# Optimization experiments

Measured on AMD Instinct MI355X. Metric: run time of the kernel, lower is better.

## Reference

```python
import jax, jax.numpy as jnp
import numpy as np

N_STATE = 1024
N_HEAD = 16
H_DIM = N_STATE // N_HEAD  # 64
NUM_ROT = 32
BASE = 10000.0
B, S = 4, 8192


def setup_inputs() -> dict:
    key = jax.random.key(0)
    k1, k2, k3 = jax.random.split(key, 3)
    x = jax.random.normal(k1, (B, S, N_STATE), dtype=jnp.float32)
    # learned params (use non-trivial values so the math is exercised)
    thetas = 0.1 * jax.random.normal(k2, (NUM_ROT,), dtype=jnp.float32)
    rotation_matrix = jnp.eye(H_DIM, dtype=jnp.float32) + 0.02 * jax.random.normal(k3, (H_DIM, H_DIM), dtype=jnp.float32)
    # buffer: inv_freq = 1 / base^(arange(0, h_dim, 2)/h_dim)
    inv_freq = 1.0 / (BASE ** (jnp.arange(0, H_DIM, 2, dtype=jnp.float32) / H_DIM))
    return {"x": x, "thetas": thetas, "rotation_matrix": rotation_matrix, "inv_freq": inv_freq}


def reference(x, thetas, rotation_matrix, inv_freq):
    batch, seq_len, n_state = x.shape
    h_dim = rotation_matrix.shape[0]
    n_head = n_state // h_dim
    num_rot = thetas.shape[0]

    xf = x.reshape(-1, h_dim)  # [B*S*n_head, h_dim]
    # Sequential Givens rotations: x @ G_k only mixes columns i and j.
    for k in range(num_rot):
        i, j = k % h_dim, (k + 1) % h_dim
        c = jnp.cos(thetas[k])
        s = jnp.sin(thetas[k])
        xi, xj = xf[:, i], xf[:, j]
        xf = xf.at[:, i].set(xi * c + xj * s).at[:, j].set(-xi * s + xj * c)
    xf = xf @ rotation_matrix
    xr = xf.reshape(batch, seq_len, n_head, h_dim)

    # RoPE-style sin/cos mixing (split-even/odd, concat halves as in source)
    pos = jnp.arange(seq_len, dtype=jnp.float32)
    sinusoid = pos[:, None] * inv_freq[None, :]          # [S, h_dim/2]
    sin = jnp.sin(sinusoid)[None, :, None, :]            # [1,S,1,h_dim/2]
    cos = jnp.cos(sinusoid)[None, :, None, :]
    x1, x2 = xr[..., ::2], xr[..., 1::2]
    out = jnp.concatenate([x1 * cos - x2 * sin, x1 * sin + x2 * cos], axis=-1)
    return out.reshape(batch, seq_len, n_state)
```

## Files before the change

kernel.cpp:

```cpp
#include <hip/hip_runtime.h>
#include <hip/hip_bf16.h>


#define TOKENS_PER_WAVE 8
#define N_TILES 32768
#define N_BLOCKS (N_TILES / (4 * TOKENS_PER_WAVE))

typedef __attribute__((ext_vector_type(8))) short short8;
typedef __attribute__((ext_vector_type(4))) float f32x4;

__device__ __forceinline__ unsigned short f2bf_bits(float f) {
  return __bfloat16_as_ushort(__float2bfloat16(f));
}

__global__ __launch_bounds__(64) void prep_kernel(
    const float* __restrict__ thetas,
    const float* __restrict__ R,
    short* __restrict__ Bws) {
  const int t = threadIdx.x;
  float col[64];
#pragma unroll
  for (int d = 0; d < 64; ++d) col[d] = R[d * 64 + t];
#pragma unroll
  for (int k = 31; k >= 0; --k) {
    float th = thetas[k];
    float ck = cosf(th), sk = sinf(th);
    float a = col[k], b = col[k + 1];
    col[k]     = ck * a - sk * b;
    col[k + 1] = sk * a + ck * b;
  }
  __shared__ float Ml[64][64];
#pragma unroll
  for (int d = 0; d < 64; ++d) Ml[d][t] = col[d];
  __syncthreads();

  short8* Bp = (short8*)Bws;
  const int cb = t & 15, kg = t >> 4;
#pragma unroll
  for (int s = 0; s < 2; ++s) {
#pragma unroll
    for (int nt = 0; nt < 4; ++nt) {
      const int c2 = cb + 16 * nt;
      const int pc = (c2 < 32) ? (2 * c2) : (2 * (c2 - 32) + 1);
      short8 hf;
#pragma unroll
      for (int e = 0; e < 8; ++e) {
        const int k = s * 32 + kg * 8 + e;
        hf[e] = (short)f2bf_bits(Ml[k][pc]);
      }
      Bp[(s * 4 + nt) * 64 + t] = hf;
    }
  }
}

__global__ __launch_bounds__(256, 4) void rope_mfma(
    const float* __restrict__ x,
    const float* __restrict__ inv_freq,
    const short* __restrict__ Bws,
    float* __restrict__ out) {
  const int lane = threadIdx.x & 63;
  const int wid = threadIdx.x >> 6;
  const int cb = lane & 15;
  const int kg = lane >> 4;

  const int tile0 = ((int)blockIdx.x * 4 + wid) * TOKENS_PER_WAVE;

  __shared__ alignas(16) float stage[4][2][16 * 64];
  __shared__ alignas(16) short8 Btab[8 * 64];

  f32x4 pb[4];
  {
    const f32x4* xb = (const f32x4*)x + (size_t)tile0 * 256;
#pragma unroll
    for (int j = 0; j < 4; ++j) pb[j] = xb[j * 64 + lane];
  }

  {
    const f32x4* Bg = (const f32x4*)Bws;
    f32x4* Bl = (f32x4*)Btab;
    const int i = threadIdx.x;
    Bl[i] = Bg[i];
    Bl[i + 256] = Bg[i + 256];
  }
  __syncthreads();

  short8 bh[8];
#pragma unroll
  for (int i = 0; i < 8; ++i) bh[i] = Btab[i * 64 + lane];

  const float iv0 = inv_freq[cb];
  const float iv1 = inv_freq[cb + 16];

#pragma unroll
  for (int t = 0; t < TOKENS_PER_WAVE; ++t) {
    const int tile = tile0 + t;
    const size_t rb = (size_t)tile * 16;
    float* st = stage[wid][t & 1];

    f32x4 va[4];
#pragma unroll
    for (int j = 0; j < 4; ++j) va[j] = pb[j];
    if (t + 1 < TOKENS_PER_WAVE) {
      const f32x4* xn = (const f32x4*)x + (size_t)(tile + 1) * 256;
#pragma unroll
      for (int j = 0; j < 4; ++j) pb[j] = xn[j * 64 + lane];
    }

    const int pos = tile & 8191;
    float sv0, cv0, sv1, cv1;
    __sincosf((float)pos * iv0, &sv0, &cv0);
    __sincosf((float)pos * iv1, &sv1, &cv1);

    {
      const int r0 = lane >> 4;
      const int c16 = lane & 15;
#pragma unroll
      for (int j = 0; j < 4; ++j) {
        const int row = j * 4 + r0;
        *(f32x4*)&st[row * 64 + (((c16 ^ row) & 15) << 2)] = va[j];
      }
    }
    asm volatile("" ::: "memory");

    float af[2][8];
#pragma unroll
    for (int s = 0; s < 2; ++s) {
#pragma unroll
      for (int t2 = 0; t2 < 2; ++t2) {
        const int ch = s * 8 + kg * 2 + t2;
        f32x4 q = *(const f32x4*)&st[cb * 64 + (((ch ^ cb) & 15) << 2)];
        af[s][t2 * 4 + 0] = q.x;
        af[s][t2 * 4 + 1] = q.y;
        af[s][t2 * 4 + 2] = q.z;
        af[s][t2 * 4 + 3] = q.w;
      }
    }

    short8 ah[2], al[2];
#pragma unroll
    for (int s = 0; s < 2; ++s) {
#pragma unroll
      for (int e = 0; e < 8; ++e) {
        float f = af[s][e];
        __hip_bfloat16 h = __float2bfloat16(f);
        ah[s][e] = (short)__bfloat16_as_ushort(h);
        al[s][e] = (short)f2bf_bits(f - __bfloat162float(h));
      }
    }

    f32x4 acc[4];
#pragma unroll
    for (int nt = 0; nt < 4; ++nt) acc[nt] = (f32x4){0.f, 0.f, 0.f, 0.f};
#pragma unroll
    for (int s = 0; s < 2; ++s) {
#pragma unroll
      for (int nt = 0; nt < 4; ++nt) {
        acc[nt] = __builtin_amdgcn_mfma_f32_16x16x32_bf16(ah[s], bh[s * 4 + nt], acc[nt], 0, 0, 0);
        acc[nt] = __builtin_amdgcn_mfma_f32_16x16x32_bf16(al[s], bh[s * 4 + nt], acc[nt], 0, 0, 0);
      }
    }

#pragma unroll
    for (int nt = 0; nt < 4; ++nt) {
      const float cvx = (nt & 1) ? cv1 : cv0;
      const float ssv = ((nt & 1) ? sv1 : sv0) * ((nt < 2) ? -1.f : 1.f);
      const int chunk = (cb >> 2) + 4 * nt;
      const int c1i = cb & 3;
#pragma unroll
      for (int r = 0; r < 4; ++r) {
        const int lrow = kg * 4 + r;
        float y = acc[nt][r];
        float p = acc[nt ^ 2][r];
        st[lrow * 64 + ((chunk ^ lrow) << 2) + c1i] = fmaf(p, ssv, y * cvx);
      }
    }
    asm volatile("s_waitcnt lgkmcnt(0)" ::: "memory");

#pragma unroll
    for (int i = 0; i < 4; ++i) {
      const int g = i * 4 + kg;
      const f32x4 v = *(const f32x4*)&st[g * 64 + ((cb ^ g) << 2)];
      __builtin_nontemporal_store(v, (f32x4*)(out + (rb + g) * 64) + cb);
    }
    asm volatile("" ::: "memory");
  }
}

extern "C" void kernel_launch(void* const* d_in, const int* in_sizes, int n_in,
                              void* d_out, int out_size, void* d_ws, size_t ws_size,
                              hipStream_t stream) {
  const float* x        = (const float*)d_in[0];
  const float* thetas   = (const float*)d_in[1];
  const float* R        = (const float*)d_in[2];
  const float* inv_freq = (const float*)d_in[3];

  prep_kernel<<<1, 64, 0, stream>>>(thetas, R, (short*)d_ws);
  rope_mfma<<<N_BLOCKS, 256, 0, stream>>>(x, inv_freq, (const short*)d_ws, (float*)d_out);
}
```

Measured before the change: 54.85 us.

## Fuse rotation-matrix prep into main kernel, recomputing per block in LDS

Removes the separate single-block prep kernel and instead has the first wave of every block build the fused Givens+rotation matrix in shared memory and convert it to the bf16 MFMA B-operand layout. This eliminates one kernel launch and the serial dependency between the two launches. In exchange, each of the 1024 blocks redoes the 64x64 matrix construction (64 global loads per thread, 32 sequential rotations with cosf/sinf, LDS transposes) before its first MFMA, adding per-block startup latency while the other three waves wait at the barrier.

```diff
diff --git a/kernel.cpp b/kernel.cpp
--- a/kernel.cpp
+++ b/kernel.cpp
@@ -13,53 +13,15 @@
   return __bfloat16_as_ushort(__float2bfloat16(f));
 }
 
-__global__ __launch_bounds__(64) void prep_kernel(
+__global__ __launch_bounds__(256, 4) void rope_mfma(
+    const float* __restrict__ x,
     const float* __restrict__ thetas,
     const float* __restrict__ R,
-    short* __restrict__ Bws) {
-  const int t = threadIdx.x;
-  float col[64];
-#pragma unroll
-  for (int d = 0; d < 64; ++d) col[d] = R[d * 64 + t];
-#pragma unroll
-  for (int k = 31; k >= 0; --k) {
-    float th = thetas[k];
-    float ck = cosf(th), sk = sinf(th);
-    float a = col[k], b = col[k + 1];
-    col[k]     = ck * a - sk * b;
-    col[k + 1] = sk * a + ck * b;
-  }
-  __shared__ float Ml[64][64];
-#pragma unroll
-  for (int d = 0; d < 64; ++d) Ml[d][t] = col[d];
-  __syncthreads();
-
-  short8* Bp = (short8*)Bws;
-  const int cb = t & 15, kg = t >> 4;
-#pragma unroll
-  for (int s = 0; s < 2; ++s) {
-#pragma unroll
-    for (int nt = 0; nt < 4; ++nt) {
-      const int c2 = cb + 16 * nt;
-      const int pc = (c2 < 32) ? (2 * c2) : (2 * (c2 - 32) + 1);
-      short8 hf;
-#pragma unroll
-      for (int e = 0; e < 8; ++e) {
-        const int k = s * 32 + kg * 8 + e;
-        hf[e] = (short)f2bf_bits(Ml[k][pc]);
-      }
-      Bp[(s * 4 + nt) * 64 + t] = hf;
-    }
-  }
-}
-
-__global__ __launch_bounds__(256, 4) void rope_mfma(
-    const float* __restrict__ x,
     const float* __restrict__ inv_freq,
-    const short* __restrict__ Bws,
     float* __restrict__ out) {
-  const int lane = threadIdx.x & 63;
-  const int wid = threadIdx.x >> 6;
+  const int tid = threadIdx.x;
+  const int lane = tid & 63;
+  const int wid = tid >> 6;
   const int cb = lane & 15;
   const int kg = lane >> 4;
 
@@ -75,12 +37,36 @@
     for (int j = 0; j < 4; ++j) pb[j] = xb[j * 64 + lane];
   }
 
-  {
-    const f32x4* Bg = (const f32x4*)Bws;
-    f32x4* Bl = (f32x4*)Btab;
-    const int i = threadIdx.x;
-    Bl[i] = Bg[i];
-    Bl[i + 256] = Bg[i + 256];
+  float* Mlf = &stage[0][0][0];
+  if (tid < 64) {
+    const int t = tid;
+#pragma unroll 4
+    for (int d = 0; d < 64; ++d) Mlf[d * 64 + t] = R[d * 64 + t];
+    asm volatile("" ::: "memory");
+    for (int k = 31; k >= 0; --k) {
+      float th = thetas[k];
+      float ck = cosf(th), sk = sinf(th);
+      float a = Mlf[k * 64 + t], b = Mlf[(k + 1) * 64 + t];
+      Mlf[k * 64 + t]       = ck * a - sk * b;
+      Mlf[(k + 1) * 64 + t] = sk * a + ck * b;
+    }
+    asm volatile("s_waitcnt lgkmcnt(0)" ::: "memory");
+    const int fcb = t & 15, fkg = t >> 4;
+#pragma unroll
+    for (int s = 0; s < 2; ++s) {
+#pragma unroll
+      for (int nt = 0; nt < 4; ++nt) {
+        const int c2 = fcb + 16 * nt;
+        const int pc = (c2 < 32) ? (2 * c2) : (2 * (c2 - 32) + 1);
+        short8 hf;
+#pragma unroll
+        for (int e = 0; e < 8; ++e) {
+          const int k = s * 32 + fkg * 8 + e;
+          hf[e] = (short)f2bf_bits(Mlf[k * 64 + pc]);
+        }
+        Btab[(s * 4 + nt) * 64 + t] = hf;
+      }
+    }
   }
   __syncthreads();
 
@@ -194,6 +180,5 @@
   const float* R        = (const float*)d_in[2];
   const float* inv_freq = (const float*)d_in[3];
 
-  prep_kernel<<<1, 64, 0, stream>>>(thetas, R, (short*)d_ws);
-  rope_mfma<<<N_BLOCKS, 256, 0, stream>>>(x, inv_freq, (const short*)d_ws, (float*)d_out);
+  rope_mfma<<<N_BLOCKS, 256, 0, stream>>>(x, thetas, R, inv_freq, (float*)d_out);
 }
```

New measurement: 53.85 us. Within noise of the previous version (-1.8%).
